# Kernel tuning notes

Hardware: AMD Instinct MI355X
Metric: run time of the kernel (lower is better)

Reference implementation:

```python
import jax, jax.numpy as jnp
import numpy as np

TOP_K = 8
DILATION = 2
KERNEL = 7
W_POS = 1.0
W_NEG = 0.1
EPS = 1e-8  # torch F.cosine_similarity eps


def unfold(x, k, d):
    # nn.Unfold(kernel_size=k, padding=(k//2)*d, dilation=d) -> [B, C, k*k, H, W]
    B, C, H, W = x.shape
    p = (k // 2) * d
    xp = jnp.pad(x, ((0, 0), (0, 0), (p, p), (p, p)))
    patches = [xp[:, :, i * d:i * d + H, j * d:j * d + W]
               for i in range(k) for j in range(k)]
    return jnp.stack(patches, axis=2)


def setup_inputs() -> dict:
    key = jax.random.key(0)
    k1, k2, k3, k4 = jax.random.split(key, 4)
    return {
        "logits_trg": jax.random.normal(k1, (2, 19, 128, 128), dtype=jnp.float32),
        "logits_ema": jax.random.normal(k2, (2, 19, 64, 64), dtype=jnp.float32),
        "x_ema": jax.random.normal(k3, (2, 64, 32, 32), dtype=jnp.float32),
        "mix_masks": jax.random.uniform(k4, (2, 1, 128, 128), dtype=jnp.float32),
    }


def reference(logits_trg, logits_ema, x_ema, mix_masks):
    B, C, H, W = logits_trg.shape
    # ignore_mask_trg = F.interpolate(1 - mix_masks, (H,W), 'nearest') > 0.5 (already at (H,W))
    ignore = (1.0 - mix_masks) > 0.5  # [B,1,H,W] bool

    # logits_ema bilinear upsample to (H,W) (align_corners=False == half-pixel)
    logits_ema_up = jax.image.resize(logits_ema, (B, C, H, W), method='bilinear')
    unf_logits = unfold(logits_ema_up, KERNEL, DILATION)  # [B,C,K,H,W], K=k^2

    # get_sim_feat: nearest upsample (integer factor == torch 'nearest') then cosine sim
    f = H // x_ema.shape[2]
    feats = jnp.repeat(jnp.repeat(x_ema, f, axis=2), f, axis=3)  # [B,Cf,H,W]
    unf_feats = unfold(feats, KERNEL, DILATION)                  # [B,Cf,K,H,W]
    dot = jnp.einsum('bckhw,bchw->bkhw', unf_feats, feats)
    n_u = jnp.maximum(jnp.sqrt(jnp.sum(unf_feats * unf_feats, axis=1)), EPS)  # [B,K,H,W]
    n_c = jnp.maximum(jnp.sqrt(jnp.sum(feats * feats, axis=1)), EPS)          # [B,H,W]
    sim_feat = dot / (n_u * n_c[:, None])  # [B,K,H,W]

    # top-k over kernel window (largest top_k+1, smallest top_k)
    sim_t = jnp.moveaxis(sim_feat, 1, -1)             # [B,H,W,K]
    vmax, imax = jax.lax.top_k(sim_t, TOP_K + 1)
    vneg, imin = jax.lax.top_k(-sim_t, TOP_K)
    vmin = -vneg

    def weighted_agg(vals, idx):
        # vals/idx: [B,H,W,t] -> weighted sum of gathered logits over window -> [B,C,H,W]
        idx = jnp.moveaxis(idx, -1, 1)    # [B,t,H,W]
        vals = jnp.moveaxis(vals, -1, 1)  # [B,t,H,W]
        t = idx.shape[1]
        idxb = jnp.broadcast_to(idx[:, None], (B, C, t, H, W))
        g = jnp.take_along_axis(unf_logits, idxb, axis=2)  # [B,C,t,H,W]
        return jnp.sum(vals[:, None] * g, axis=2)

    pl_pos = jax.nn.softmax(weighted_agg(vmax, imax), axis=1)
    pl_neg = jax.nn.softmax(weighted_agg(vmin, imin), axis=1)

    def bce_with_logits(x, z):
        # -(z*log(sig(x)) + (1-z)*log(1-sig(x))) = (1-z)*x - log_sigmoid(x)
        return (1.0 - z) * x - jax.nn.log_sigmoid(x)

    m = ignore.astype(logits_trg.dtype)  # [B,1,H,W]
    denom = jnp.sum(m) * C               # mask repeated across C classes
    loss_pos = jnp.sum(bce_with_logits(logits_trg, pl_pos) * m) / denom
    loss_neg = jnp.sum(-bce_with_logits(logits_trg, pl_neg) * m) / denom
    return jnp.stack([loss_pos * W_POS, loss_neg * W_NEG])
```

## Files before the change

### kernel.cpp

```cpp
#include <hip/hip_runtime.h>
#include <math.h>

#define NB 2
#define NC 19
#define NH 128
#define NW 128
#define NCF 64
#define NHE 64
#define NHX 32
#define EPSC 1e-8f
#define NBLK 512

#define WS_PART_OFF 64

__device__ __forceinline__ int clampi(int v, int lo, int hi) {
    return v < lo ? lo : (v > hi ? hi : v);
}

__global__ __launch_bounds__(256) void pfst_main(
    const float* __restrict__ trg, const float* __restrict__ ema,
    const float* __restrict__ xe,  const float* __restrict__ mix,
    float* __restrict__ part)
{
    __shared__ float se[NC * 217];
    __shared__ float sx[NCF * 49];
    __shared__ float scn3[3 * 48];
    __shared__ float red[4][3];

    int tid = threadIdx.x;
    int l = tid & 3;
    int u = tid & 7;
    int lc = l & 1;
    bool posH = (l < 2);
    int q = tid >> 2;
    int bid = blockIdx.x;
    int b = bid >> 8;
    int rem = bid & 255;
    int h0 = ((rem >> 2) << 1);
    int w0 = (rem & 3) << 5;
    int h = h0 + (q >> 5);
    int w = w0 + (q & 31);

    int eyB = (h0 - 7) >> 1, exB = (w0 - 7) >> 1;
    int by0 = (h0 - 6) >> 2, bx0 = (w0 - 6) >> 2;

    float xreg[12];
    {
        const float* Xb = xe + b * (NCF * NHX * NHX);
        #pragma unroll
        for (int r = 0; r < 12; r++) {
            int idx = tid + r * 256;
            int ch = idx / 48; int rr = idx - ch * 48;
            int a = rr / 12;   int d = rr - a * 12;
            int gy = clampi(by0 + a, 0, 31), gx = clampi(bx0 + d, 0, 31);
            xreg[r] = Xb[ch * (NHX * NHX) + gy * 32 + gx];
        }
    }
    float ereg[17];
    {
        const float* Eb = ema + b * NC * (NHE * NHE);
        #pragma unroll
        for (int r = 0; r < 17; r++) {
            int idx = tid + r * 256;
            if (idx < NC * 216) {
                int c = idx / 216; int rr = idx - c * 216;
                int rw = rr / 24;  int x = rr - rw * 24;
                int gy = clampi(eyB + rw, 0, 63), gx = clampi(exB + x, 0, 63);
                ereg[r] = Eb[c * (NHE * NHE) + gy * 64 + gx];
            } else ereg[r] = 0.f;
        }
    }
    #pragma unroll
    for (int r = 0; r < 12; r++) {
        int idx = tid + r * 256;
        int ch = idx / 48; int rr = idx - ch * 48;
        sx[ch * 49 + rr] = xreg[r];
    }
    __syncthreads();

    if (tid < 144) {
        int cell = tid % 48;
        int chunk = tid / 48;
        int ch0 = chunk * 21;
        int nch = (chunk == 2) ? 22 : 21;
        float s = 0.f;
        #pragma unroll
        for (int cc = 0; cc < 22; cc++) {
            if (cc < nch) {
                float v = sx[(ch0 + cc) * 49 + cell];
                s = fmaf(v, v, s);
            }
        }
        scn3[chunk * 48 + cell] = s;
    }
    __syncthreads();

    float mval = mix[(b << 14) + (h << 7) + w];
    bool active = mval < 0.5f;
    float af = active ? 1.f : 0.f;
    af += __shfl_xor(af, 4);
    bool apair = (af > 0.f);

    float lp = 0.f, ln = 0.f;
    float cm = (active && l == 0) ? 1.f : 0.f;

    float tx[10];
    float vsel[9]; int isel[9];

    if (active) {
        const float* Tb = trg + b * NC * (NH * NW) + (h << 7) + w;
        #pragma unroll
        for (int jc = 0; jc < 10; jc++) {
            int c = lc + 2 * jc;
            tx[jc] = (c < NC) ? Tb[c * (NH * NW)] : 0.f;
        }
    }

    if (apair) {
        int bx = (w - 6) >> 2;
        int trow[4], tcol[4];
        #pragma unroll
        for (int a = 0; a < 4; a++) trow[a] = clampi(by0 + a, 0, 31) - by0;
        #pragma unroll
        for (int d = 0; d < 4; d++) tcol[d] = clampi(bx + d, 0, 31) - bx0;
        int coffT = ((h >> 2) - by0) * 12 + ((w >> 2) - bx0);

        float dotc[16];
        #pragma unroll
        for (int e = 0; e < 16; e++) dotc[e] = 0.f;

        #pragma unroll
        for (int cc = 0; cc < 8; cc++) {
            const float* Sx = sx + (u * 8 + cc) * 49;
            float cv = Sx[coffT];
            #pragma unroll
            for (int a = 0; a < 4; a++) {
                int rb = trow[a] * 12;
                #pragma unroll
                for (int d = 0; d < 4; d++)
                    dotc[a * 4 + d] = fmaf(Sx[rb + tcol[d]], cv, dotc[a * 4 + d]);
            }
        }
        #pragma unroll
        for (int e = 0; e < 16; e++) {
            dotc[e] += __shfl_xor(dotc[e], 1);
            dotc[e] += __shfl_xor(dotc[e], 2);
            dotc[e] += __shfl_xor(dotc[e], 4);
        }

        float cn_c = (scn3[coffT] + scn3[48 + coffT]) + scn3[96 + coffT];
        float nc2 = 1.f / fmaxf(sqrtf(cn_c), EPSC);
        float scell[16];
        #pragma unroll
        for (int a = 0; a < 4; a++) {
            #pragma unroll
            for (int d = 0; d < 4; d++) {
                int x = trow[a] * 12 + tcol[d];
                float cn_u = (scn3[x] + scn3[48 + x]) + scn3[96 + x];
                float nu = fmaxf(sqrtf(cn_u), EPSC);
                scell[a * 4 + d] = dotc[a * 4 + d] * nc2 / nu;
            }
        }

        const int QA[7] = {0, 0, 1, 1, 2, 2, 3};
        const int QB[7] = {0, 1, 1, 2, 2, 3, 3};
        bool ry = (h & 3) >= 2, rx = (w & 3) >= 2;
        bool posScan = (u < 4);

        float sims[49];
        #pragma unroll
        for (int i = 0; i < 7; i++) {
            int py = h + 2 * i - 6;
            bool vy = (unsigned)py < 128u;
            float srow[4];
            #pragma unroll
            for (int d = 0; d < 4; d++)
                srow[d] = ry ? scell[QA[i] * 4 + d] : scell[QB[i] * 4 + d];
            #pragma unroll
            for (int j = 0; j < 7; j++) {
                int px = w + 2 * j - 6;
                bool vx = (unsigned)px < 128u;
                float v = rx ? srow[QA[j]] : srow[QB[j]];
                float sv = (vy && vx) ? v : 0.f;
                sims[i * 7 + j] = posScan ? sv : -sv;
            }
        }

        int s4 = u & 3;
        float hv[13];
        #pragma unroll
        for (int kk = 0; kk < 13; kk++) {
            float v0 = (kk < 12) ? sims[kk]      : -3.4e38f;
            float v1 = (kk < 12) ? sims[12 + kk] : -3.4e38f;
            float v2 = (kk < 12) ? sims[24 + kk] : -3.4e38f;
            float v3 = sims[36 + kk];
            float lo = (s4 & 1) ? v1 : v0;
            float hi = (s4 & 1) ? v3 : v2;
            hv[kk] = (s4 & 2) ? hi : lo;
        }
        int k0 = s4 * 12;
        int nown = (s4 == 3) ? 13 : 12;
        {
            unsigned mymask = 0u;
            #pragma unroll
            for (int t = 0; t < 9; t++) {
                float best = -3.4e38f; int bkk = 20;
                #pragma unroll
                for (int kk = 0; kk < 13; kk++) {
                    if (!((mymask >> kk) & 1u) && hv[kk] > best) { best = hv[kk]; bkk = kk; }
                }
                int bi = k0 + bkk;
                #pragma unroll
                for (int st = 1; st <= 2; st <<= 1) {
                    float ov = __shfl_xor(best, st);
                    int   oi = __shfl_xor(bi, st);
                    if (ov > best || (ov == best && oi < bi)) { best = ov; bi = oi; }
                }
                vsel[t] = best; isel[t] = bi;
                int rel = bi - k0;
                if ((unsigned)rel < (unsigned)nown) mymask |= 1u << rel;
            }
        }

        bool useOwn = ((u < 4) == (l < 2));
        #pragma unroll
        for (int t = 0; t < 9; t++) {
            float ov = __shfl_xor(vsel[t], 4);
            int   oi = __shfl_xor(isel[t], 4);
            vsel[t] = useOwn ? vsel[t] : ov;
            isel[t] = useOwn ? isel[t] : oi;
        }
    }

    #pragma unroll
    for (int r = 0; r < 17; r++) {
        int idx = tid + r * 256;
        if (idx < NC * 216) {
            int c = idx / 216; int rr = idx - c * 216;
            se[c * 217 + rr] = ereg[r];
        }
    }
    __syncthreads();

    if (active) {
        float av[10];
        #pragma unroll
        for (int jc = 0; jc < 10; jc++) av[jc] = 0.f;

        #pragma unroll
        for (int t = 0; t < 9; t++) {
            if (posH || t < 8) {
                int k = isel[t];
                float val = posH ? vsel[t] : -vsel[t];
                int i = (k * 586) >> 12; int j = k - 7 * i;
                int py = h + 2 * i - 6, px = w + 2 * j - 6;
                if ((unsigned)py < 128u && (unsigned)px < 128u) {
                    int iy0 = (py - 1) >> 1; float ty = (py & 1) ? 0.25f : 0.75f;
                    int ix0 = (px - 1) >> 1; float txx = (px & 1) ? 0.25f : 0.75f;
                    int y0 = clampi(iy0, 0, 63), y1 = clampi(iy0 + 1, 0, 63);
                    int x0 = clampi(ix0, 0, 63), x1 = clampi(ix0 + 1, 0, 63);
                    float w00 = (1.f - ty) * (1.f - txx), w01 = (1.f - ty) * txx;
                    float w10 = ty * (1.f - txx),         w11 = ty * txx;
                    int o00 = (y0 - eyB) * 24 + (x0 - exB), o01 = (y0 - eyB) * 24 + (x1 - exB);
                    int o10 = (y1 - eyB) * 24 + (x0 - exB), o11 = (y1 - eyB) * 24 + (x1 - exB);
                    #pragma unroll
                    for (int jc = 0; jc < 10; jc++) {
                        int c = lc + 2 * jc;
                        if (c < NC) {
                            const float* Sc = se + c * 217;
                            float g = w00 * Sc[o00] + w01 * Sc[o01]
                                    + w10 * Sc[o10] + w11 * Sc[o11];
                            av[jc] = fmaf(val, g, av[jc]);
                        }
                    }
                }
            }
        }

        float m = -3.4e38f;
        #pragma unroll
        for (int jc = 0; jc < 10; jc++) {
            int c = lc + 2 * jc;
            if (c < NC) m = fmaxf(m, av[jc]);
        }
        m = fmaxf(m, __shfl_xor(m, 1));

        float Z = 0.f, S = 0.f, Bs = 0.f;
        #pragma unroll
        for (int jc = 0; jc < 10; jc++) {
            int c = lc + 2 * jc;
            if (c < NC) {
                float x = tx[jc];
                float e = expf(av[jc] - m); Z += e; S += e * x;
                float ls = fminf(x, 0.f) - log1pf(expf(-fabsf(x)));
                Bs += x - ls;
            }
        }
        Z += __shfl_xor(Z, 1); S += __shfl_xor(S, 1); Bs += __shfl_xor(Bs, 1);

        float res = posH ? (Bs - S / Z) : (S / Z - Bs);
        float oth = __shfl_xor(res, 2);
        lp = (l == 0) ? res : 0.f;
        ln = (l == 0) ? oth : 0.f;
    }

    #pragma unroll
    for (int off = 32; off > 0; off >>= 1) {
        lp += __shfl_down(lp, off);
        ln += __shfl_down(ln, off);
        cm += __shfl_down(cm, off);
    }
    int wid = tid >> 6;
    if ((tid & 63) == 0) { red[wid][0] = lp; red[wid][1] = ln; red[wid][2] = cm; }
    __syncthreads();
    if (tid == 0) {
        float* pb = part + 3 * blockIdx.x;
        pb[0] = red[0][0] + red[1][0] + red[2][0] + red[3][0];
        pb[1] = red[0][1] + red[1][1] + red[2][1] + red[3][1];
        pb[2] = red[0][2] + red[1][2] + red[2][2] + red[3][2];
    }
}

__global__ __launch_bounds__(256) void pfst_final(const float* __restrict__ part,
                                                  float* __restrict__ out) {
    int t = threadIdx.x;
    float lp = part[3 * t + 0] + part[3 * (t + 256) + 0];
    float ln = part[3 * t + 1] + part[3 * (t + 256) + 1];
    float cm = part[3 * t + 2] + part[3 * (t + 256) + 2];
    #pragma unroll
    for (int off = 32; off > 0; off >>= 1) {
        lp += __shfl_down(lp, off);
        ln += __shfl_down(ln, off);
        cm += __shfl_down(cm, off);
    }
    __shared__ float red[4][3];
    int wid = t >> 6;
    if ((t & 63) == 0) { red[wid][0] = lp; red[wid][1] = ln; red[wid][2] = cm; }
    __syncthreads();
    if (t == 0) {
        float a0 = red[0][0] + red[1][0] + red[2][0] + red[3][0];
        float a1 = red[0][1] + red[1][1] + red[2][1] + red[3][1];
        float a2 = red[0][2] + red[1][2] + red[2][2] + red[3][2];
        float denom = a2 * (float)NC;
        out[0] = a0 / denom;
        out[1] = a1 / denom * 0.1f;
    }
}

extern "C" void kernel_launch(void* const* d_in, const int* in_sizes, int n_in,
                              void* d_out, int out_size, void* d_ws, size_t ws_size,
                              hipStream_t stream) {
    const float* trg = (const float*)d_in[0];
    const float* ema = (const float*)d_in[1];
    const float* xe  = (const float*)d_in[2];
    const float* mix = (const float*)d_in[3];
    float* part = (float*)((char*)d_ws + WS_PART_OFF);
    float* out  = (float*)d_out;

    hipLaunchKernelGGL(pfst_main, dim3(NBLK), dim3(256), 0, stream,
                       trg, ema, xe, mix, part);
    hipLaunchKernelGGL(pfst_final, dim3(1), dim3(256), 0, stream, part, out);
}
```

Measured before the change: 31.09 us.

## Use eight threads per pixel and smaller 2x16 tiles across 1024 blocks

Each pixel now gets 8 lanes instead of 4, and each block covers a 2x16 tile instead of 2x32, doubling the grid to 1024 blocks. Per-thread work shrinks: feature dot-product channels per lane fall from 8 to 4, the top-k scan covers 6-7 candidates per lane instead of 12-13, and each lane handles 5 classes in the aggregation instead of 10. Shared-memory halos shrink, but halo overhead per output pixel grows, and the extra shuffle stages add cross-lane traffic. The final reduction now loops over the larger partial count.

```diff
diff --git a/kernel.cpp b/kernel.cpp
--- a/kernel.cpp
+++ b/kernel.cpp
@@ -9,9 +9,11 @@
 #define NHE 64
 #define NHX 32
 #define EPSC 1e-8f
-#define NBLK 512
+#define NBLK 1024
 
 #define WS_PART_OFF 64
+
+#define NEGINF -3.4e38f
 
 __device__ __forceinline__ int clampi(int v, int lo, int hi) {
     return v < lo ? lo : (v > hi ? hi : v);
@@ -22,96 +24,93 @@
     const float* __restrict__ xe,  const float* __restrict__ mix,
     float* __restrict__ part)
 {
-    __shared__ float se[NC * 217];
-    __shared__ float sx[NCF * 49];
-    __shared__ float scn3[3 * 48];
+    __shared__ float se[NC * 145];
+    __shared__ float sx[NCF * 33];
+    __shared__ float scn4[4 * 32];
     __shared__ float red[4][3];
 
     int tid = threadIdx.x;
-    int l = tid & 3;
-    int u = tid & 7;
-    int lc = l & 1;
-    bool posH = (l < 2);
-    int q = tid >> 2;
+    int u8 = tid & 7;
+    int g16 = tid & 15;
+    int lc4 = u8 & 3;
+    bool posH = (u8 < 4);
+    int q = tid >> 3;
     int bid = blockIdx.x;
-    int b = bid >> 8;
-    int rem = bid & 255;
-    int h0 = ((rem >> 2) << 1);
-    int w0 = (rem & 3) << 5;
-    int h = h0 + (q >> 5);
-    int w = w0 + (q & 31);
+    int b = bid >> 9;
+    int rem = bid & 511;
+    int h0 = (rem >> 3) << 1;
+    int w0 = (rem & 7) << 4;
+    int h = h0 + (q >> 4);
+    int w = w0 + (q & 15);
 
     int eyB = (h0 - 7) >> 1, exB = (w0 - 7) >> 1;
     int by0 = (h0 - 6) >> 2, bx0 = (w0 - 6) >> 2;
 
-    float xreg[12];
+    float xreg[8];
     {
         const float* Xb = xe + b * (NCF * NHX * NHX);
         #pragma unroll
-        for (int r = 0; r < 12; r++) {
+        for (int r = 0; r < 8; r++) {
             int idx = tid + r * 256;
-            int ch = idx / 48; int rr = idx - ch * 48;
-            int a = rr / 12;   int d = rr - a * 12;
+            int ch = idx >> 5; int rr = idx & 31;
+            int a = rr >> 3;   int d = rr & 7;
             int gy = clampi(by0 + a, 0, 31), gx = clampi(bx0 + d, 0, 31);
             xreg[r] = Xb[ch * (NHX * NHX) + gy * 32 + gx];
         }
     }
-    float ereg[17];
+    float ereg[11];
     {
         const float* Eb = ema + b * NC * (NHE * NHE);
         #pragma unroll
-        for (int r = 0; r < 17; r++) {
+        for (int r = 0; r < 11; r++) {
             int idx = tid + r * 256;
-            if (idx < NC * 216) {
-                int c = idx / 216; int rr = idx - c * 216;
-                int rw = rr / 24;  int x = rr - rw * 24;
+            if (idx < NC * 144) {
+                int c = idx / 144; int rr = idx - c * 144;
+                int rw = rr >> 4;  int x = rr & 15;
                 int gy = clampi(eyB + rw, 0, 63), gx = clampi(exB + x, 0, 63);
                 ereg[r] = Eb[c * (NHE * NHE) + gy * 64 + gx];
             } else ereg[r] = 0.f;
         }
     }
     #pragma unroll
-    for (int r = 0; r < 12; r++) {
+    for (int r = 0; r < 8; r++) {
         int idx = tid + r * 256;
-        int ch = idx / 48; int rr = idx - ch * 48;
-        sx[ch * 49 + rr] = xreg[r];
-    }
-    __syncthreads();
-
-    if (tid < 144) {
-        int cell = tid % 48;
-        int chunk = tid / 48;
-        int ch0 = chunk * 21;
-        int nch = (chunk == 2) ? 22 : 21;
+        int ch = idx >> 5; int rr = idx & 31;
+        sx[ch * 33 + rr] = xreg[r];
+    }
+    __syncthreads();
+
+    if (tid < 128) {
+        int cell = tid & 31;
+        int chunk = tid >> 5;
+        int ch0 = chunk * 16;
         float s = 0.f;
         #pragma unroll
-        for (int cc = 0; cc < 22; cc++) {
-            if (cc < nch) {
-                float v = sx[(ch0 + cc) * 49 + cell];
-                s = fmaf(v, v, s);
-            }
-        }
-        scn3[chunk * 48 + cell] = s;
+        for (int cc = 0; cc < 16; cc++) {
+            float v = sx[(ch0 + cc) * 33 + cell];
+            s = fmaf(v, v, s);
+        }
+        scn4[chunk * 32 + cell] = s;
     }
     __syncthreads();
 
     float mval = mix[(b << 14) + (h << 7) + w];
     bool active = mval < 0.5f;
     float af = active ? 1.f : 0.f;
-    af += __shfl_xor(af, 4);
+    af += __shfl_xor(af, 8);
     bool apair = (af > 0.f);
 
     float lp = 0.f, ln = 0.f;
-    float cm = (active && l == 0) ? 1.f : 0.f;
-
-    float tx[10];
+    float cm = (active && u8 == 0) ? 1.f : 0.f;
+
+    float tx[5];
     float vsel[9]; int isel[9];
 
     if (active) {
         const float* Tb = trg + b * NC * (NH * NW) + (h << 7) + w;
         #pragma unroll
-        for (int jc = 0; jc < 10; jc++) {
-            int c = lc + 2 * jc;
+        for (int jc = 0; jc < 5; jc++) {
+            int c = lc4 + 4 * jc;
             tx[jc] = (c < NC) ? Tb[c * (NH * NW)] : 0.f;
         }
     }
@@ -123,19 +122,19 @@
         for (int a = 0; a < 4; a++) trow[a] = clampi(by0 + a, 0, 31) - by0;
         #pragma unroll
         for (int d = 0; d < 4; d++) tcol[d] = clampi(bx + d, 0, 31) - bx0;
-        int coffT = ((h >> 2) - by0) * 12 + ((w >> 2) - bx0);
+        int coffT = ((h >> 2) - by0) * 8 + ((w >> 2) - bx0);
 
         float dotc[16];
         #pragma unroll
         for (int e = 0; e < 16; e++) dotc[e] = 0.f;
 
         #pragma unroll
-        for (int cc = 0; cc < 8; cc++) {
-            const float* Sx = sx + (u * 8 + cc) * 49;
+        for (int cc = 0; cc < 4; cc++) {
+            const float* Sx = sx + (g16 * 4 + cc) * 33;
             float cv = Sx[coffT];
             #pragma unroll
             for (int a = 0; a < 4; a++) {
-                int rb = trow[a] * 12;
+                int rb = trow[a] * 8;
                 #pragma unroll
                 for (int d = 0; d < 4; d++)
                     dotc[a * 4 + d] = fmaf(Sx[rb + tcol[d]], cv, dotc[a * 4 + d]);
@@ -146,17 +145,18 @@
             dotc[e] += __shfl_xor(dotc[e], 1);
             dotc[e] += __shfl_xor(dotc[e], 2);
             dotc[e] += __shfl_xor(dotc[e], 4);
-        }
-
-        float cn_c = (scn3[coffT] + scn3[48 + coffT]) + scn3[96 + coffT];
+            dotc[e] += __shfl_xor(dotc[e], 8);
+        }
+
+        float cn_c = ((scn4[coffT] + scn4[32 + coffT]) + scn4[64 + coffT]) + scn4[96 + coffT];
         float nc2 = 1.f / fmaxf(sqrtf(cn_c), EPSC);
         float scell[16];
         #pragma unroll
         for (int a = 0; a < 4; a++) {
             #pragma unroll
             for (int d = 0; d < 4; d++) {
-                int x = trow[a] * 12 + tcol[d];
-                float cn_u = (scn3[x] + scn3[48 + x]) + scn3[96 + x];
+                int x = trow[a] * 8 + tcol[d];
+                float cn_u = ((scn4[x] + scn4[32 + x]) + scn4[64 + x]) + scn4[96 + x];
                 float nu = fmaxf(sqrtf(cn_u), EPSC);
                 scell[a * 4 + d] = dotc[a * 4 + d] * nc2 / nu;
             }
@@ -165,7 +165,7 @@
         const int QA[7] = {0, 0, 1, 1, 2, 2, 3};
         const int QB[7] = {0, 1, 1, 2, 2, 3, 3};
         bool ry = (h & 3) >= 2, rx = (w & 3) >= 2;
-        bool posScan = (u < 4);
+        bool posScan = (g16 < 8);
 
         float sims[49];
         #pragma unroll
@@ -186,32 +186,41 @@
             }
         }
 
-        int s4 = u & 3;
-        float hv[13];
-        #pragma unroll
-        for (int kk = 0; kk < 13; kk++) {
-            float v0 = (kk < 12) ? sims[kk]      : -3.4e38f;
-            float v1 = (kk < 12) ? sims[12 + kk] : -3.4e38f;
-            float v2 = (kk < 12) ? sims[24 + kk] : -3.4e38f;
-            float v3 = sims[36 + kk];
-            float lo = (s4 & 1) ? v1 : v0;
-            float hi = (s4 & 1) ? v3 : v2;
-            hv[kk] = (s4 & 2) ? hi : lo;
-        }
-        int k0 = s4 * 12;
-        int nown = (s4 == 3) ? 13 : 12;
+        int s8 = g16 & 7;
+        int k0 = s8 * 6;
+        int nown = (s8 == 7) ? 7 : 6;
+        float hv[7];
+        #pragma unroll
+        for (int kk = 0; kk < 7; kk++) {
+            float c0 = (kk < 6) ? sims[kk]      : NEGINF;
+            float c1 = (kk < 6) ? sims[6 + kk]  : NEGINF;
+            float c2 = (kk < 6) ? sims[12 + kk] : NEGINF;
+            float c3 = (kk < 6) ? sims[18 + kk] : NEGINF;
+            float c4 = (kk < 6) ? sims[24 + kk] : NEGINF;
+            float c5 = (kk < 6) ? sims[30 + kk] : NEGINF;
+            float c6 = (kk < 6) ? sims[36 + kk] : NEGINF;
+            float c7 = sims[42 + kk];
+            float t01 = (s8 & 1) ? c1 : c0;
+            float t23 = (s8 & 1) ? c3 : c2;
+            float t45 = (s8 & 1) ? c5 : c4;
+            float t67 = (s8 & 1) ? c7 : c6;
+            float u0 = (s8 & 2) ? t23 : t01;
+            float u1 = (s8 & 2) ? t67 : t45;
+            float vv = (s8 & 4) ? u1 : u0;
+            hv[kk] = (kk >= nown) ? NEGINF : vv;
+        }
         {
             unsigned mymask = 0u;
             #pragma unroll
             for (int t = 0; t < 9; t++) {
-                float best = -3.4e38f; int bkk = 20;
+                float best = NEGINF; int bkk = 10;
                 #pragma unroll
-                for (int kk = 0; kk < 13; kk++) {
+                for (int kk = 0; kk < 7; kk++) {
                     if (!((mymask >> kk) & 1u) && hv[kk] > best) { best = hv[kk]; bkk = kk; }
                 }
                 int bi = k0 + bkk;
                 #pragma unroll
-                for (int st = 1; st <= 2; st <<= 1) {
+                for (int st = 1; st <= 4; st <<= 1) {
                     float ov = __shfl_xor(best, st);
                     int   oi = __shfl_xor(bi, st);
                     if (ov > best || (ov == best && oi < bi)) { best = ov; bi = oi; }
@@ -222,30 +231,30 @@
             }
         }
 
-        bool useOwn = ((u < 4) == (l < 2));
+        bool useOwn = ((g16 < 8) == (u8 < 4));
         #pragma unroll
         for (int t = 0; t < 9; t++) {
-            float ov = __shfl_xor(vsel[t], 4);
-            int   oi = __shfl_xor(isel[t], 4);
+            float ov = __shfl_xor(vsel[t], 8);
+            int   oi = __shfl_xor(isel[t], 8);
             vsel[t] = useOwn ? vsel[t] : ov;
             isel[t] = useOwn ? isel[t] : oi;
         }
     }
 
     #pragma unroll
-    for (int r = 0; r < 17; r++) {
+    for (int r = 0; r < 11; r++) {
         int idx = tid + r * 256;
-        if (idx < NC * 216) {
-            int c = idx / 216; int rr = idx - c * 216;
-            se[c * 217 + rr] = ereg[r];
+        if (idx < NC * 144) {
+            int c = idx / 144; int rr = idx - c * 144;
+            se[c * 145 + rr] = ereg[r];
         }
     }
     __syncthreads();
 
     if (active) {
-        float av[10];
-        #pragma unroll
-        for (int jc = 0; jc < 10; jc++) av[jc] = 0.f;
+        float av[5];
+        #pragma unroll
+        for (int jc = 0; jc < 5; jc++) av[jc] = 0.f;
 
         #pragma unroll
         for (int t = 0; t < 9; t++) {
@@ -261,13 +270,13 @@
                     int x0 = clampi(ix0, 0, 63), x1 = clampi(ix0 + 1, 0, 63);
                     float w00 = (1.f - ty) * (1.f - txx), w01 = (1.f - ty) * txx;
                     float w10 = ty * (1.f - txx),         w11 = ty * txx;
-                    int o00 = (y0 - eyB) * 24 + (x0 - exB), o01 = (y0 - eyB) * 24 + (x1 - exB);
-                    int o10 = (y1 - eyB) * 24 + (x0 - exB), o11 = (y1 - eyB) * 24 + (x1 - exB);
+                    int o00 = (y0 - eyB) * 16 + (x0 - exB), o01 = (y0 - eyB) * 16 + (x1 - exB);
+                    int o10 = (y1 - eyB) * 16 + (x0 - exB), o11 = (y1 - eyB) * 16 + (x1 - exB);
                     #pragma unroll
-                    for (int jc = 0; jc < 10; jc++) {
-                        int c = lc + 2 * jc;
+                    for (int jc = 0; jc < 5; jc++) {
+                        int c = lc4 + 4 * jc;
                         if (c < NC) {
-                            const float* Sc = se + c * 217;
+                            const float* Sc = se + c * 145;
                             float g = w00 * Sc[o00] + w01 * Sc[o01]
                                     + w10 * Sc[o10] + w11 * Sc[o11];
                             av[jc] = fmaf(val, g, av[jc]);
@@ -277,18 +286,18 @@
             }
         }
 
-        float m = -3.4e38f;
-        #pragma unroll
-        for (int jc = 0; jc < 10; jc++) {
-            int c = lc + 2 * jc;
+        float m = NEGINF;
+        #pragma unroll
+        for (int jc = 0; jc < 5; jc++) {
+            int c = lc4 + 4 * jc;
             if (c < NC) m = fmaxf(m, av[jc]);
         }
-        m = fmaxf(m, __shfl_xor(m, 1));
+        m = fmaxf(m, __shfl_xor(m, 1)); m = fmaxf(m, __shfl_xor(m, 2));
 
         float Z = 0.f, S = 0.f, Bs = 0.f;
         #pragma unroll
-        for (int jc = 0; jc < 10; jc++) {
-            int c = lc + 2 * jc;
+        for (int jc = 0; jc < 5; jc++) {
+            int c = lc4 + 4 * jc;
             if (c < NC) {
                 float x = tx[jc];
                 float e = expf(av[jc] - m); Z += e; S += e * x;
@@ -296,12 +305,15 @@
                 Bs += x - ls;
             }
         }
-        Z += __shfl_xor(Z, 1); S += __shfl_xor(S, 1); Bs += __shfl_xor(Bs, 1);
+        #pragma unroll
+        for (int s = 1; s <= 2; s <<= 1) {
+            Z += __shfl_xor(Z, s); S += __shfl_xor(S, s); Bs += __shfl_xor(Bs, s);
+        }
 
         float res = posH ? (Bs - S / Z) : (S / Z - Bs);
-        float oth = __shfl_xor(res, 2);
-        lp = (l == 0) ? res : 0.f;
-        ln = (l == 0) ? oth : 0.f;
+        float oth = __shfl_xor(res, 4);
+        lp = (u8 == 0) ? res : 0.f;
+        ln = (u8 == 0) ? oth : 0.f;
     }
 
     #pragma unroll
@@ -324,9 +336,14 @@
 __global__ __launch_bounds__(256) void pfst_final(const float* __restrict__ part,
                                                   float* __restrict__ out) {
     int t = threadIdx.x;
-    float lp = part[3 * t + 0] + part[3 * (t + 256) + 0];
-    float ln = part[3 * t + 1] + part[3 * (t + 256) + 1];
-    float cm = part[3 * t + 2] + part[3 * (t + 256) + 2];
+    float lp = 0.f, ln = 0.f, cm = 0.f;
+    #pragma unroll
+    for (int rpt = 0; rpt < NBLK / 256; rpt++) {
+        int idx = t + rpt * 256;
+        lp += part[3 * idx + 0];
+        ln += part[3 * idx + 1];
+        cm += part[3 * idx + 2];
+    }
     #pragma unroll
     for (int off = 32; off > 0; off >>= 1) {
         lp += __shfl_down(lp, off);
```

After: 34.76 us. 11.8% more time.
